# Optimization experiments

Hardware: AMD Instinct MI355X
Metric: run time of the kernel (lower is better)

Reference implementation:

```python
import jax, jax.numpy as jnp
import numpy as np

ROPE_BASE = 1000000.0
EPS = 1e-6
N_HEADS = 8


def apply_rope(x, base=ROPE_BASE):
    # x: [b, s, h, d]
    b, s, h, d = x.shape
    half = d // 2
    theta = 1.0 / base ** (2 * jnp.arange(half) / d)          # [half]
    angles = jnp.arange(s)[:, None] * theta[None, :]          # [s, half]
    cos = jnp.cos(angles)[None, :, None, :]                   # [1, s, 1, half]
    sin = jnp.sin(angles)[None, :, None, :]
    x1, x2 = jnp.split(x, 2, axis=-1)
    return jnp.concatenate([x1 * cos - x2 * sin, x1 * sin + x2 * cos], axis=-1)


def setup_inputs() -> dict:
    key = jax.random.key(0)
    ks = jax.random.split(key, 5)
    b, s, dim = 2, 4096, 512
    x = jax.random.normal(ks[0], (b, s, dim), dtype=jnp.float32)
    scale = jnp.ones((dim,), dtype=jnp.float32)
    init = 1.0 / np.sqrt(dim)
    Wq = jax.random.normal(ks[1], (dim, dim), dtype=jnp.float32) * init
    Wk = jax.random.normal(ks[2], (dim, dim), dtype=jnp.float32) * init
    Wv = jax.random.normal(ks[3], (dim, dim), dtype=jnp.float32) * init
    Wo = jax.random.normal(ks[4], (dim, dim), dtype=jnp.float32) * init
    return {"x": x, "scale": scale, "Wq": Wq, "Wk": Wk, "Wv": Wv, "Wo": Wo}


def reference(x, scale, Wq, Wk, Wv, Wo):
    b, s, dim = x.shape
    h = N_HEADS
    dh = dim // h
    # RMSNorm (use_fast_variance=False path)
    variance = jnp.mean(x ** 2, axis=-1, keepdims=True)
    x_norm = x / jnp.sqrt(variance + EPS) * scale
    # Projections (flax Linear: y = x @ kernel, kernel [in, out])
    q = (x_norm @ Wq).reshape(b, s, h, dh)
    k = (x_norm @ Wk).reshape(b, s, h, dh)
    v = (x_norm @ Wv).reshape(b, s, h, dh)
    q = apply_rope(q)
    k = apply_rope(k)
    scores = jnp.einsum('bthd,bshd->bhts', q, k) / jnp.sqrt(jnp.float32(dh))
    mask = jnp.triu(jnp.full((s, s), -jnp.inf, dtype=jnp.float32), k=1)
    scores = scores + mask[None, None, :, :]
    attn = jax.nn.softmax(scores, axis=-1)
    out = jnp.einsum('bhts,bshd->bthd', attn, v).reshape(b, s, dim)
    return out @ Wo
```

## Files before the change

### kernel.cpp

```cpp
#include <hip/hip_runtime.h>
#include <hip/hip_bf16.h>

typedef _Float16 f16;
typedef _Float16 f16x4 __attribute__((ext_vector_type(4)));
typedef _Float16 f16x8 __attribute__((ext_vector_type(8)));
typedef float f32x4 __attribute__((ext_vector_type(4)));

#define S_LEN 4096
#define DIM   512
#define NH    8
#define DH    64
#define BATCH 2
#define BHDIM (BATCH*NH)

#define QSCALE 0.18033688011112042f

__device__ __forceinline__ void gld16(const f16* g, f16* l) {
#if __has_builtin(__builtin_amdgcn_global_load_lds)
  __builtin_amdgcn_global_load_lds((const __attribute__((address_space(1))) void*)g,
                                   (__attribute__((address_space(3))) void*)l, 16, 0, 0);
#else
  *(f16x8*)l = *(const f16x8*)g;
#endif
}

__device__ __forceinline__ float fexp2(float x) {
#if __has_builtin(__builtin_amdgcn_exp2f)
  return __builtin_amdgcn_exp2f(x);
#else
  return exp2f(x);
#endif
}

__global__ __launch_bounds__(256) void rmsnorm_kernel(
    const float* __restrict__ x, const float* __restrict__ scale,
    f16* __restrict__ xn) {
  int row = blockIdx.x;
  int tid = threadIdx.x;
  const float* xr = x + (size_t)row * DIM;
  float2 v = *(const float2*)(xr + tid*2);
  float ss = v.x*v.x + v.y*v.y;
  #pragma unroll
  for (int off = 32; off > 0; off >>= 1) ss += __shfl_down(ss, off);
  __shared__ float red[4];
  if ((tid & 63) == 0) red[tid >> 6] = ss;
  __syncthreads();
  float tot = red[0] + red[1] + red[2] + red[3];
  float inv = rsqrtf(tot * (1.0f/DIM) + 1e-6f);
  float2 s = *(const float2*)(scale + tid*2);
  xn[(size_t)row*DIM + tid*2+0] = (f16)(v.x*inv*s.x);
  xn[(size_t)row*DIM + tid*2+1] = (f16)(v.y*inv*s.y);
}

__global__ void transpose_kernel(const float* __restrict__ Wq,
                                 const float* __restrict__ Wk,
                                 const float* __restrict__ Wv,
                                 const float* __restrict__ Wo,
                                 f16* __restrict__ wt_qkv, f16* __restrict__ wo_t) {
  __shared__ f16 tile[32][33];
  int mat = blockIdx.z;
  const float* src = (mat == 0) ? Wq : (mat == 1) ? Wk : (mat == 2) ? Wv : Wo;
  f16* dst = (mat < 3) ? (wt_qkv + (size_t)mat*DIM*DIM) : wo_t;
  int k0 = blockIdx.y * 32, n0 = blockIdx.x * 32;
  int tx = threadIdx.x, ty = threadIdx.y;
  #pragma unroll
  for (int i = 0; i < 32; i += 8)
    tile[ty+i][tx] = (f16)src[(size_t)(k0+ty+i)*DIM + n0+tx];
  __syncthreads();
  #pragma unroll
  for (int i = 0; i < 32; i += 8)
    dst[(size_t)(n0+ty+i)*DIM + k0+tx] = tile[tx][ty+i];
}

__global__ __launch_bounds__(256) void rope_table_kernel(float* __restrict__ ctab,
                                                         float* __restrict__ stab) {
  int idx = blockIdx.x*256 + threadIdx.x;
  int t = idx >> 5, d = idx & 31;
  float theta = exp2f(-(float)d * (19.931568569324174f / 32.0f));
  float sv, cv;
  sincosf((float)t * theta, &sv, &cv);
  ctab[idx] = cv; stab[idx] = sv;
}

__device__ __forceinline__ void gemm128_acc(
    const f16* __restrict__ A, const f16* __restrict__ Bt,
    int m0, int n0, f16* As, f16* Bs, f32x4 (&acc)[4][4]) {
  const int tid = threadIdx.x;
  const int wave = tid >> 6, lane = tid & 63;
  const int l16 = lane & 15, quad = lane >> 4;
  const int mrow = (wave & 1) * 64, ncol = (wave >> 1) * 64;
  const int srow = tid >> 3;
  const int gc = (tid & 7) ^ ((tid >> 3) & 7);

  for (int k0 = 0; k0 < DIM; k0 += 64) {
    if (k0) __syncthreads();
    #pragma unroll
    for (int i = 0; i < 4; i++) {
      gld16(A  + (size_t)(m0 + i*32 + srow)*DIM + k0 + gc*8, As + i*2048 + tid*8);
      gld16(Bt + (size_t)(n0 + i*32 + srow)*DIM + k0 + gc*8, Bs + i*2048 + tid*8);
    }
    __syncthreads();
    #pragma unroll
    for (int kc = 0; kc < 2; kc++) {
      f16x8 a[4], b[4];
      #pragma unroll
      for (int mt = 0; mt < 4; mt++) {
        int row = mrow + mt*16 + l16;
        a[mt] = *(const f16x8*)(As + row*64 + (((quad + 4*kc) ^ (l16 & 7)) * 8));
      }
      #pragma unroll
      for (int nt = 0; nt < 4; nt++) {
        int row = ncol + nt*16 + l16;
        b[nt] = *(const f16x8*)(Bs + row*64 + (((quad + 4*kc) ^ (l16 & 7)) * 8));
      }
      #pragma unroll
      for (int mt = 0; mt < 4; mt++)
        #pragma unroll
        for (int nt = 0; nt < 4; nt++)
          acc[mt][nt] = __builtin_amdgcn_mfma_f32_16x16x32_f16(a[mt], b[nt], acc[mt][nt], 0, 0, 0);
    }
  }
}

__global__ __launch_bounds__(256) void qkv_gemm_kernel(
    const f16* __restrict__ xn, const f16* __restrict__ wt,
    const float* __restrict__ ctab, const float* __restrict__ stab,
    f16* __restrict__ qbuf, f16* __restrict__ kbuf, f16* __restrict__ vt) {
  __shared__ __align__(16) f16 As[128*64], Bs[128*64];
  int m0 = blockIdx.x * 128, n0 = blockIdx.y * 128;
  f32x4 acc[4][4] = {};
  gemm128_acc(xn, wt, m0, n0, As, Bs, acc);

  const int tid = threadIdx.x;
  const int wave = tid >> 6, lane = tid & 63;
  const int l16 = lane & 15, quad = lane >> 4;
  int ncol = n0 + (wave >> 1) * 64;
  int which = ncol >> 9;
  int head = (ncol >> 6) & 7;
  int mbase = m0 + (wave & 1) * 64;

  if (which <= 1) {
    #pragma unroll
    for (int mt = 0; mt < 4; mt++)
      #pragma unroll
      for (int nt = 0; nt < 2; nt++) {
        int d = nt*16 + l16;
        #pragma unroll
        for (int r = 0; r < 4; r++) {
          int t = (mbase + mt*16 + quad*4 + r) & 4095;
          float cv = ctab[t*32 + d], sv = stab[t*32 + d];
          float x1 = acc[mt][nt][r], x2 = acc[mt][nt+2][r];
          acc[mt][nt][r]   = x1*cv - x2*sv;
          acc[mt][nt+2][r] = x1*sv + x2*cv;
        }
      }
  }
  if (which < 2) {
    float osc = (which == 0) ? QSCALE : 1.0f;
    f16* dst = which ? kbuf : qbuf;
    #pragma unroll
    for (int mt = 0; mt < 4; mt++)
      #pragma unroll
      for (int nt = 0; nt < 4; nt++)
        #pragma unroll
        for (int r = 0; r < 4; r++) {
          int m = mbase + mt*16 + quad*4 + r;
          int b = m >> 12, t = m & 4095;
          dst[(((size_t)(b*NH + head))*S_LEN + t)*DH + nt*16 + l16] = (f16)(acc[mt][nt][r]*osc);
        }
  } else {
    #pragma unroll
    for (int mt = 0; mt < 4; mt++)
      #pragma unroll
      for (int nt = 0; nt < 4; nt++) {
        int m = mbase + mt*16 + quad*4;
        int b = m >> 12, t = m & 4095;
        int d = nt*16 + l16;
        f16x4 v4 = {(f16)acc[mt][nt][0], (f16)acc[mt][nt][1],
                    (f16)acc[mt][nt][2], (f16)acc[mt][nt][3]};
        *(f16x4*)(vt + ((size_t)((b*NH + head)*DH + d))*S_LEN + t) = v4;
      }
  }
}

__global__ __launch_bounds__(128, 2) void attn_kernel(
    const f16* __restrict__ qbuf, const f16* __restrict__ kbuf,
    const f16* __restrict__ vtb, f16* __restrict__ ao) {
  int bid = blockIdx.x;
  int bh  = bid & 15;
  int p   = bid >> 4;

  int tid = threadIdx.x;
  int wave = tid >> 6, lane = tid & 63;
  int l16 = lane & 15, quad = lane >> 4;

  const f16* Q = qbuf + (size_t)bh*S_LEN*DH;
  const f16* K = kbuf + (size_t)bh*S_LEN*DH;
  const f16* V = vtb  + (size_t)bh*DH*S_LEN;

  int bandv[2] = {127 - p, p};
  int tcnt[2]  = {((127 - p) >> 1) + 1, (p >> 1) + 1};
  int rbase[2] = {bandv[0]*32 + wave*16, bandv[1]*32 + wave*16};

  f16x8 qa[2][2];
  #pragma unroll
  for (int bi = 0; bi < 2; bi++) {
    const f16* qrow = Q + (size_t)(rbase[bi] + l16)*DH + quad*8;
    qa[bi][0] = *(const f16x8*)(qrow);
    qa[bi][1] = *(const f16x8*)(qrow + 32);
  }

  f32x4 o[2][4] = {};
  float m_i[2] = {-1e30f, -1e30f};
  float l_i[2] = {0.f, 0.f};

  __shared__ __align__(16) f16 kt[2*4096];
  __shared__ __align__(16) f16 vs[2*4096];
  __shared__ __align__(16) f16 pls[4096];

  const int gcs = (tid & 7) ^ ((tid >> 3) & 7);
  const int srow = tid >> 3;

  #define STAGE(buf, kv)                                                        \
    do {                                                                        \
      f16* ktb = kt + (buf)*4096;                                               \
      f16* vsb = vs + (buf)*4096;                                               \
      _Pragma("unroll")                                                         \
      for (int n = 0; n < 4; n++) {                                             \
        gld16(K + (size_t)((kv) + n*16 + srow)*DH + gcs*8, ktb + n*1024 + tid*8);\
        gld16(V + (size_t)(n*16 + srow)*S_LEN + (kv) + gcs*8, vsb + n*1024 + tid*8);\
      }                                                                         \
    } while (0)

  STAGE(0, 0);
  __syncthreads();

  int nth = tcnt[0];
  for (int it = 0; it < nth; ++it) {
    int kv0 = it * 64;
    int cur = it & 1;
    if (it + 1 < nth) STAGE(cur ^ 1, kv0 + 64);

    const f16* ktc = kt + cur*4096;
    const f16* vsc = vs + cur*4096;

    bool act1 = (it < tcnt[1]);
    bool dia[2] = {it == tcnt[0] - 1, it == tcnt[1] - 1};

    #pragma unroll
    for (int bi = 0; bi < 2; bi++) {
      if (bi == 1 && !act1) continue;
      bool diag = dia[bi];
      int ntl = diag ? ((bandv[bi] & 1) ? 4 : 2) : 4;

      f32x4 st[4];
      #pragma unroll
      for (int nt = 0; nt < 4; nt++) {
        if (nt >= ntl) continue;
        int row = nt*16 + l16;
        f16x8 kf0 = *(const f16x8*)(ktc + row*64 + (((quad)     ^ (row & 7))*8));
        f16x8 kf1 = *(const f16x8*)(ktc + row*64 + (((quad + 4) ^ (row & 7))*8));
        f32x4 z = {};
        z = __builtin_amdgcn_mfma_f32_16x16x32_f16(kf0, qa[bi][0], z, 0, 0, 0);
        st[nt] = __builtin_amdgcn_mfma_f32_16x16x32_f16(kf1, qa[bi][1], z, 0, 0, 0);
      }

      int qglob = rbase[bi] + l16;
      float rmx = -1e30f;
      #pragma unroll
      for (int nt = 0; nt < 4; nt++) {
        if (nt >= ntl) continue;
        if (diag) {
          int kb = kv0 + nt*16 + quad*4;
          #pragma unroll
          for (int r = 0; r < 4; r++) {
            float v = st[nt][r];
            if (kb + r > qglob) v = -1e30f;
            st[nt][r] = v;
            rmx = fmaxf(rmx, v);
          }
        } else {
          #pragma unroll
          for (int r = 0; r < 4; r++) rmx = fmaxf(rmx, st[nt][r]);
        }
      }
      rmx = fmaxf(rmx, __shfl_xor(rmx, 16));
      rmx = fmaxf(rmx, __shfl_xor(rmx, 32));
      if (!__all(rmx <= m_i[bi] + 8.0f)) {
        float mnew = fmaxf(m_i[bi], rmx);
        float alpha = fexp2(m_i[bi] - mnew);
        m_i[bi] = mnew;
        float al[4];
        #pragma unroll
        for (int r = 0; r < 4; r++) al[r] = __shfl(alpha, quad*4 + r);
        #pragma unroll
        for (int dnt = 0; dnt < 4; dnt++)
          #pragma unroll
          for (int r = 0; r < 4; r++) o[bi][dnt][r] *= al[r];
        l_i[bi] *= alpha;
      }
      float mref = m_i[bi];
      float rs = 0.f;
      f16* plw = pls + wave*2048 + bi*1024 + l16*64;
      #pragma unroll
      for (int nt = 0; nt < 4; nt++) {
        if (nt >= ntl) continue;
        f16x4 p4;
        #pragma unroll
        for (int r = 0; r < 4; r++) {
          float pv = fexp2(st[nt][r] - mref);
          rs += pv;
          p4[r] = (f16)pv;
        }
        int cw = nt*2 + (quad >> 1);
        *(f16x4*)(plw + ((cw ^ (l16 & 7))*8) + (quad & 1)*4) = p4;
      }
      rs += __shfl_xor(rs, 16);
      rs += __shfl_xor(rs, 32);
      l_i[bi] += rs;
    }

    int kcl0 = dia[0] ? ((bandv[0] & 1) ? 2 : 1) : 2;
    int kcl1 = act1 ? (dia[1] ? ((bandv[1] & 1) ? 2 : 1) : 2) : 0;
    #pragma unroll
    for (int kc = 0; kc < 2; kc++) {
      bool lv0 = (kc < kcl0), lv1 = (kc < kcl1);
      if (!lv0 && !lv1) continue;
      int cp = ((kc*4 + quad) ^ (l16 & 7))*8;
      f16x8 pa0, pa1;
      if (lv0) pa0 = *(const f16x8*)(pls + wave*2048 +        l16*64 + cp);
      if (lv1) pa1 = *(const f16x8*)(pls + wave*2048 + 1024 + l16*64 + cp);
      #pragma unroll
      for (int dnt = 0; dnt < 4; dnt++) {
        int vr = dnt*16 + l16;
        f16x8 vf = *(const f16x8*)(vsc + vr*64 + (((kc*4 + quad) ^ (vr & 7))*8));
        if (lv0) o[0][dnt] = __builtin_amdgcn_mfma_f32_16x16x32_f16(pa0, vf, o[0][dnt], 0, 0, 0);
        if (lv1) o[1][dnt] = __builtin_amdgcn_mfma_f32_16x16x32_f16(pa1, vf, o[1][dnt], 0, 0, 0);
      }
    }

    __syncthreads();
  }
  #undef STAGE

  int b = bh >> 3, h = bh & 7;
  #pragma unroll
  for (int bi = 0; bi < 2; bi++) {
    float lr[4];
    #pragma unroll
    for (int r = 0; r < 4; r++) lr[r] = __shfl(l_i[bi], quad*4 + r);
    #pragma unroll
    for (int r = 0; r < 4; r++) {
      float invl = 1.0f / lr[r];
      int t = rbase[bi] + quad*4 + r;
      size_t rowoff = ((size_t)(b*S_LEN + t))*DIM + h*DH;
      #pragma unroll
      for (int dnt = 0; dnt < 4; dnt++)
        ao[rowoff + dnt*16 + l16] = (f16)(o[bi][dnt][r]*invl);
    }
  }
}

__global__ __launch_bounds__(256) void out_gemm_kernel(
    const f16* __restrict__ ao, const f16* __restrict__ wot,
    float* __restrict__ out) {
  __shared__ __align__(16) f16 As[128*64], Bs[128*64];
  int m0 = blockIdx.x * 128, n0 = blockIdx.y * 128;
  f32x4 acc[4][4] = {};
  gemm128_acc(ao, wot, m0, n0, As, Bs, acc);

  const int tid = threadIdx.x;
  const int wave = tid >> 6, lane = tid & 63;
  const int l16 = lane & 15, quad = lane >> 4;
  int ncol = n0 + (wave >> 1) * 64;
  int mbase = m0 + (wave & 1) * 64;
  #pragma unroll
  for (int mt = 0; mt < 4; mt++)
    #pragma unroll
    for (int nt = 0; nt < 4; nt++)
      #pragma unroll
      for (int r = 0; r < 4; r++)
        out[(size_t)(mbase + mt*16 + quad*4 + r)*DIM + ncol + nt*16 + l16] = acc[mt][nt][r];
}

extern "C" void kernel_launch(void* const* d_in, const int* in_sizes, int n_in,
                              void* d_out, int out_size, void* d_ws, size_t ws_size,
                              hipStream_t stream) {
  const float* x     = (const float*)d_in[0];
  const float* scale = (const float*)d_in[1];
  const float* Wq    = (const float*)d_in[2];
  const float* Wk    = (const float*)d_in[3];
  const float* Wv    = (const float*)d_in[4];
  const float* Wo    = (const float*)d_in[5];
  float* out = (float*)d_out;

  const size_t ROWS = (size_t)BATCH * S_LEN;
  char* ws = (char*)d_ws;
  f16* xn     = (f16*)ws;  ws += ROWS * DIM * sizeof(f16);
  f16* wt_qkv = (f16*)ws;  ws += (size_t)3 * DIM * DIM * sizeof(f16);
  f16* wo_t   = (f16*)ws;  ws += (size_t)DIM * DIM * sizeof(f16);
  f16* qb     = (f16*)ws;  ws += (size_t)BHDIM * S_LEN * DH * sizeof(f16);
  f16* kb     = (f16*)ws;  ws += (size_t)BHDIM * S_LEN * DH * sizeof(f16);
  f16* vt     = (f16*)ws;  ws += (size_t)BHDIM * S_LEN * DH * sizeof(f16);
  float* ctab = (float*)ws; ws += (size_t)S_LEN * 32 * sizeof(float);
  float* stab = (float*)ws; ws += (size_t)S_LEN * 32 * sizeof(float);
  f16* ao     = xn;

  size_t need = (size_t)(ws - (char*)d_ws);
  if (ws_size < need) return;

  rmsnorm_kernel   <<<ROWS, 256, 0, stream>>>(x, scale, xn);
  transpose_kernel <<<dim3(16,16,4), dim3(32,8), 0, stream>>>(Wq, Wk, Wv, Wo, wt_qkv, wo_t);
  rope_table_kernel<<<512, 256, 0, stream>>>(ctab, stab);
  qkv_gemm_kernel  <<<dim3(64,12), 256, 0, stream>>>(xn, wt_qkv, ctab, stab, qb, kb, vt);
  attn_kernel      <<<1024, 128, 0, stream>>>(qb, kb, vt, ao);
  out_gemm_kernel  <<<dim3(64,4), 256, 0, stream>>>(ao, wo_t, out);
}
```

Before: 211.0 us.

## Stage K/V through registers into single LDS buffer and raise occupancy

Replaces the double-buffered direct global-to-LDS K/V staging with register prefetch of the next tile, written into a single LDS buffer after the compute finishes. The P tile buffer is halved by running the PV product per band right after each softmax instead of after both bands. Together this shrinks shared memory so launch bounds can ask for 4 blocks per CU instead of 2. The trade-off is an extra barrier per iteration, more VGPR pressure from the prefetch registers, and less interleaving of the two bands' MFMAs.

```diff
diff --git a/kernel.cpp b/kernel.cpp
--- a/kernel.cpp
+++ b/kernel.cpp
@@ -183,7 +183,7 @@
   }
 }
 
-__global__ __launch_bounds__(128, 2) void attn_kernel(
+__global__ __launch_bounds__(128, 4) void attn_kernel(
     const f16* __restrict__ qbuf, const f16* __restrict__ kbuf,
     const f16* __restrict__ vtb, f16* __restrict__ ao) {
   int bid = blockIdx.x;
@@ -214,35 +214,36 @@
   float m_i[2] = {-1e30f, -1e30f};
   float l_i[2] = {0.f, 0.f};
 
-  __shared__ __align__(16) f16 kt[2*4096];
-  __shared__ __align__(16) f16 vs[2*4096];
-  __shared__ __align__(16) f16 pls[4096];
+  __shared__ __align__(16) f16 kt[4096];
+  __shared__ __align__(16) f16 vs[4096];
+  __shared__ __align__(16) f16 pls[2048];
 
   const int gcs = (tid & 7) ^ ((tid >> 3) & 7);
   const int srow = tid >> 3;
 
-  #define STAGE(buf, kv)                                                        \
-    do {                                                                        \
-      f16* ktb = kt + (buf)*4096;                                               \
-      f16* vsb = vs + (buf)*4096;                                               \
-      _Pragma("unroll")                                                         \
+  f16x8 pk[4], pvr[4];
+  #define LOADREG(kv)                                                           \
+    do { _Pragma("unroll")                                                      \
       for (int n = 0; n < 4; n++) {                                             \
-        gld16(K + (size_t)((kv) + n*16 + srow)*DH + gcs*8, ktb + n*1024 + tid*8);\
-        gld16(V + (size_t)(n*16 + srow)*S_LEN + (kv) + gcs*8, vsb + n*1024 + tid*8);\
-      }                                                                         \
-    } while (0)
-
-  STAGE(0, 0);
+        pk[n]  = *(const f16x8*)(K + (size_t)((kv) + n*16 + srow)*DH + gcs*8);  \
+        pvr[n] = *(const f16x8*)(V + (size_t)(n*16 + srow)*S_LEN + (kv) + gcs*8);\
+      } } while (0)
+  #define WRITELDS()                                                            \
+    do { _Pragma("unroll")                                                      \
+      for (int n = 0; n < 4; n++) {                                             \
+        *(f16x8*)(kt + n*1024 + tid*8) = pk[n];                                 \
+        *(f16x8*)(vs + n*1024 + tid*8) = pvr[n];                                \
+      } } while (0)
+
+  LOADREG(0);
+  WRITELDS();
   __syncthreads();
 
   int nth = tcnt[0];
   for (int it = 0; it < nth; ++it) {
     int kv0 = it * 64;
-    int cur = it & 1;
-    if (it + 1 < nth) STAGE(cur ^ 1, kv0 + 64);
-
-    const f16* ktc = kt + cur*4096;
-    const f16* vsc = vs + cur*4096;
+    bool have_next = (it + 1 < nth);
+    if (have_next) LOADREG(kv0 + 64);
 
     bool act1 = (it < tcnt[1]);
     bool dia[2] = {it == tcnt[0] - 1, it == tcnt[1] - 1};
@@ -258,8 +259,8 @@
       for (int nt = 0; nt < 4; nt++) {
         if (nt >= ntl) continue;
         int row = nt*16 + l16;
-        f16x8 kf0 = *(const f16x8*)(ktc + row*64 + (((quad)     ^ (row & 7))*8));
-        f16x8 kf1 = *(const f16x8*)(ktc + row*64 + (((quad + 4) ^ (row & 7))*8));
+        f16x8 kf0 = *(const f16x8*)(kt + row*64 + (((quad)     ^ (row & 7))*8));
+        f16x8 kf1 = *(const f16x8*)(kt + row*64 + (((quad + 4) ^ (row & 7))*8));
         f32x4 z = {};
         z = __builtin_amdgcn_mfma_f32_16x16x32_f16(kf0, qa[bi][0], z, 0, 0, 0);
         st[nt] = __builtin_amdgcn_mfma_f32_16x16x32_f16(kf1, qa[bi][1], z, 0, 0, 0);
@@ -301,7 +302,7 @@
       }
       float mref = m_i[bi];
       float rs = 0.f;
-      f16* plw = pls + wave*2048 + bi*1024 + l16*64;
+      f16* plw = pls + wave*1024 + l16*64;
       #pragma unroll
       for (int nt = 0; nt < 4; nt++) {
         if (nt >= ntl) continue;
@@ -318,30 +319,29 @@
       rs += __shfl_xor(rs, 16);
       rs += __shfl_xor(rs, 32);
       l_i[bi] += rs;
+
+      int kcl = diag ? ((bandv[bi] & 1) ? 2 : 1) : 2;
+      #pragma unroll
+      for (int kc = 0; kc < 2; kc++) {
+        if (kc >= kcl) continue;
+        f16x8 pa = *(const f16x8*)(plw - l16*64 + l16*64 + (((kc*4 + quad) ^ (l16 & 7))*8));
+        #pragma unroll
+        for (int dnt = 0; dnt < 4; dnt++) {
+          int vr = dnt*16 + l16;
+          f16x8 vf = *(const f16x8*)(vs + vr*64 + (((kc*4 + quad) ^ (vr & 7))*8));
+          o[bi][dnt] = __builtin_amdgcn_mfma_f32_16x16x32_f16(pa, vf, o[bi][dnt], 0, 0, 0);
+        }
+      }
     }
 
-    int kcl0 = dia[0] ? ((bandv[0] & 1) ? 2 : 1) : 2;
-    int kcl1 = act1 ? (dia[1] ? ((bandv[1] & 1) ? 2 : 1) : 2) : 0;
-    #pragma unroll
-    for (int kc = 0; kc < 2; kc++) {
-      bool lv0 = (kc < kcl0), lv1 = (kc < kcl1);
-      if (!lv0 && !lv1) continue;
-      int cp = ((kc*4 + quad) ^ (l16 & 7))*8;
-      f16x8 pa0, pa1;
-      if (lv0) pa0 = *(const f16x8*)(pls + wave*2048 +        l16*64 + cp);
-      if (lv1) pa1 = *(const f16x8*)(pls + wave*2048 + 1024 + l16*64 + cp);
-      #pragma unroll
-      for (int dnt = 0; dnt < 4; dnt++) {
-        int vr = dnt*16 + l16;
-        f16x8 vf = *(const f16x8*)(vsc + vr*64 + (((kc*4 + quad) ^ (vr & 7))*8));
-        if (lv0) o[0][dnt] = __builtin_amdgcn_mfma_f32_16x16x32_f16(pa0, vf, o[0][dnt], 0, 0, 0);
-        if (lv1) o[1][dnt] = __builtin_amdgcn_mfma_f32_16x16x32_f16(pa1, vf, o[1][dnt], 0, 0, 0);
-      }
+    if (have_next) {
+      __syncthreads();
+      WRITELDS();
+      __syncthreads();
     }
-
-    __syncthreads();
-  }
-  #undef STAGE
+  }
+  #undef LOADREG
+  #undef WRITELDS
 
   int b = bh >> 3, h = bh & 7;
   #pragma unroll
```

Result: slower. 545.1 us (+158.4%).

## Keep softmax probabilities in registers instead of round-tripping through LDS

Applied to the files above, without the earlier changes.

The P tile from the QK^T MFMA is now packed straight into registers (packed f16 conversion) and used as the A operand of the PV MFMA. It no longer goes through a shared-memory scratch buffer. To make the register layout match, the V fragment is gathered from LDS as two 4-element halves in a permuted k-order. The row-sum reduction across lanes is deferred to the epilogue. The QK^T loop is also merged across both bands so the K fragments load once. This removes LDS writes and reads and frees 8KB of LDS, at the cost of extra LDS read instructions for V, more register pressure, and round-toward-zero f16 conversion.

```diff
diff --git a/kernel.cpp b/kernel.cpp
--- a/kernel.cpp
+++ b/kernel.cpp
@@ -2,6 +2,7 @@
 #include <hip/hip_bf16.h>
 
 typedef _Float16 f16;
+typedef _Float16 f16x2 __attribute__((ext_vector_type(2)));
 typedef _Float16 f16x4 __attribute__((ext_vector_type(4)));
 typedef _Float16 f16x8 __attribute__((ext_vector_type(8)));
 typedef float f32x4 __attribute__((ext_vector_type(4)));
@@ -29,6 +30,16 @@
   return __builtin_amdgcn_exp2f(x);
 #else
   return exp2f(x);
+#endif
+}
+
+__device__ __forceinline__ f16x2 pk2(float a, float b) {
+#if __has_builtin(__builtin_amdgcn_cvt_pkrtz)
+  auto r = __builtin_amdgcn_cvt_pkrtz(a, b);
+  f16x2 o; __builtin_memcpy(&o, &r, sizeof(o));
+  return o;
+#else
+  f16x2 r; r[0] = (f16)a; r[1] = (f16)b; return r;
 #endif
 }
 
@@ -216,7 +227,6 @@
 
   __shared__ __align__(16) f16 kt[2*4096];
   __shared__ __align__(16) f16 vs[2*4096];
-  __shared__ __align__(16) f16 pls[4096];
 
   const int gcs = (tid & 7) ^ ((tid >> 3) & 7);
   const int srow = tid >> 3;
@@ -245,26 +255,37 @@
     const f16* vsc = vs + cur*4096;
 
     bool act1 = (it < tcnt[1]);
-    bool dia[2] = {it == tcnt[0] - 1, it == tcnt[1] - 1};
-
-    #pragma unroll
-    for (int bi = 0; bi < 2; bi++) {
-      if (bi == 1 && !act1) continue;
-      bool diag = dia[bi];
-      int ntl = diag ? ((bandv[bi] & 1) ? 4 : 2) : 4;
-
-      f32x4 st[4];
-      #pragma unroll
-      for (int nt = 0; nt < 4; nt++) {
-        if (nt >= ntl) continue;
+    bool dia0 = (it == tcnt[0] - 1), dia1 = (it == tcnt[1] - 1);
+    int ntl0 = dia0 ? ((bandv[0] & 1) ? 4 : 2) : 4;
+    int ntl1 = act1 ? (dia1 ? ((bandv[1] & 1) ? 4 : 2) : 4) : 0;
+
+    f32x4 st[2][4];
+    #pragma unroll
+    for (int nt = 0; nt < 4; nt++) {
+      bool n0 = (nt < ntl0), n1 = (nt < ntl1);
+      if (n0 || n1) {
         int row = nt*16 + l16;
         f16x8 kf0 = *(const f16x8*)(ktc + row*64 + (((quad)     ^ (row & 7))*8));
         f16x8 kf1 = *(const f16x8*)(ktc + row*64 + (((quad + 4) ^ (row & 7))*8));
-        f32x4 z = {};
-        z = __builtin_amdgcn_mfma_f32_16x16x32_f16(kf0, qa[bi][0], z, 0, 0, 0);
-        st[nt] = __builtin_amdgcn_mfma_f32_16x16x32_f16(kf1, qa[bi][1], z, 0, 0, 0);
-      }
-
+        if (n0) {
+          f32x4 z = {};
+          z = __builtin_amdgcn_mfma_f32_16x16x32_f16(kf0, qa[0][0], z, 0, 0, 0);
+          st[0][nt] = __builtin_amdgcn_mfma_f32_16x16x32_f16(kf1, qa[0][1], z, 0, 0, 0);
+        }
+        if (n1) {
+          f32x4 z = {};
+          z = __builtin_amdgcn_mfma_f32_16x16x32_f16(kf0, qa[1][0], z, 0, 0, 0);
+          st[1][nt] = __builtin_amdgcn_mfma_f32_16x16x32_f16(kf1, qa[1][1], z, 0, 0, 0);
+        }
+      }
+    }
+
+    f16x8 pa[2][2];
+    #pragma unroll
+    for (int bi = 0; bi < 2; bi++) {
+      int ntl = bi ? ntl1 : ntl0;
+      if (ntl == 0) continue;
+      bool diag = bi ? dia1 : dia0;
       int qglob = rbase[bi] + l16;
       float rmx = -1e30f;
       #pragma unroll
@@ -274,14 +295,14 @@
           int kb = kv0 + nt*16 + quad*4;
           #pragma unroll
           for (int r = 0; r < 4; r++) {
-            float v = st[nt][r];
+            float v = st[bi][nt][r];
             if (kb + r > qglob) v = -1e30f;
-            st[nt][r] = v;
+            st[bi][nt][r] = v;
             rmx = fmaxf(rmx, v);
           }
         } else {
           #pragma unroll
-          for (int r = 0; r < 4; r++) rmx = fmaxf(rmx, st[nt][r]);
+          for (int r = 0; r < 4; r++) rmx = fmaxf(rmx, st[bi][nt][r]);
         }
       }
       rmx = fmaxf(rmx, __shfl_xor(rmx, 16));
@@ -300,42 +321,42 @@
         l_i[bi] *= alpha;
       }
       float mref = m_i[bi];
+      int kcl = ntl >> 1;
       float rs = 0.f;
-      f16* plw = pls + wave*2048 + bi*1024 + l16*64;
-      #pragma unroll
-      for (int nt = 0; nt < 4; nt++) {
-        if (nt >= ntl) continue;
-        f16x4 p4;
-        #pragma unroll
-        for (int r = 0; r < 4; r++) {
-          float pv = fexp2(st[nt][r] - mref);
-          rs += pv;
-          p4[r] = (f16)pv;
-        }
-        int cw = nt*2 + (quad >> 1);
-        *(f16x4*)(plw + ((cw ^ (l16 & 7))*8) + (quad & 1)*4) = p4;
-      }
-      rs += __shfl_xor(rs, 16);
-      rs += __shfl_xor(rs, 32);
+      #pragma unroll
+      for (int c = 0; c < 2; c++) {
+        if (c >= kcl) continue;
+        float e0 = fexp2(st[bi][2*c  ][0] - mref);
+        float e1 = fexp2(st[bi][2*c  ][1] - mref);
+        float e2 = fexp2(st[bi][2*c  ][2] - mref);
+        float e3 = fexp2(st[bi][2*c  ][3] - mref);
+        float e4 = fexp2(st[bi][2*c+1][0] - mref);
+        float e5 = fexp2(st[bi][2*c+1][1] - mref);
+        float e6 = fexp2(st[bi][2*c+1][2] - mref);
+        float e7 = fexp2(st[bi][2*c+1][3] - mref);
+        rs += ((e0+e1)+(e2+e3)) + ((e4+e5)+(e6+e7));
+        f16x4 h0 = __builtin_shufflevector(pk2(e0,e1), pk2(e2,e3), 0,1,2,3);
+        f16x4 h1 = __builtin_shufflevector(pk2(e4,e5), pk2(e6,e7), 0,1,2,3);
+        pa[bi][c] = __builtin_shufflevector(h0, h1, 0,1,2,3,4,5,6,7);
+      }
       l_i[bi] += rs;
     }
 
-    int kcl0 = dia[0] ? ((bandv[0] & 1) ? 2 : 1) : 2;
-    int kcl1 = act1 ? (dia[1] ? ((bandv[1] & 1) ? 2 : 1) : 2) : 0;
-    #pragma unroll
-    for (int kc = 0; kc < 2; kc++) {
-      bool lv0 = (kc < kcl0), lv1 = (kc < kcl1);
+    int kcl0 = ntl0 >> 1, kcl1 = ntl1 >> 1;
+    #pragma unroll
+    for (int c = 0; c < 2; c++) {
+      bool lv0 = (c < kcl0), lv1 = (c < kcl1);
       if (!lv0 && !lv1) continue;
-      int cp = ((kc*4 + quad) ^ (l16 & 7))*8;
-      f16x8 pa0, pa1;
-      if (lv0) pa0 = *(const f16x8*)(pls + wave*2048 +        l16*64 + cp);
-      if (lv1) pa1 = *(const f16x8*)(pls + wave*2048 + 1024 + l16*64 + cp);
       #pragma unroll
       for (int dnt = 0; dnt < 4; dnt++) {
         int vr = dnt*16 + l16;
-        f16x8 vf = *(const f16x8*)(vsc + vr*64 + (((kc*4 + quad) ^ (vr & 7))*8));
-        if (lv0) o[0][dnt] = __builtin_amdgcn_mfma_f32_16x16x32_f16(pa0, vf, o[0][dnt], 0, 0, 0);
-        if (lv1) o[1][dnt] = __builtin_amdgcn_mfma_f32_16x16x32_f16(pa1, vf, o[1][dnt], 0, 0, 0);
+        int iLo = vr*64 + (((c*4 +     (quad>>1)) ^ (vr & 7))*8) + (quad & 1)*4;
+        int iHi = vr*64 + (((c*4 + 2 + (quad>>1)) ^ (vr & 7))*8) + (quad & 1)*4;
+        f16x4 lo = *(const f16x4*)(vsc + iLo);
+        f16x4 hi = *(const f16x4*)(vsc + iHi);
+        f16x8 vf = __builtin_shufflevector(lo, hi, 0,1,2,3,4,5,6,7);
+        if (lv0) o[0][dnt] = __builtin_amdgcn_mfma_f32_16x16x32_f16(pa[0][c], vf, o[0][dnt], 0, 0, 0);
+        if (lv1) o[1][dnt] = __builtin_amdgcn_mfma_f32_16x16x32_f16(pa[1][c], vf, o[1][dnt], 0, 0, 0);
       }
     }
 
@@ -346,9 +367,12 @@
   int b = bh >> 3, h = bh & 7;
   #pragma unroll
   for (int bi = 0; bi < 2; bi++) {
+    float lf = l_i[bi];
+    lf += __shfl_xor(lf, 16);
+    lf += __shfl_xor(lf, 32);
     float lr[4];
     #pragma unroll
-    for (int r = 0; r < 4; r++) lr[r] = __shfl(l_i[bi], quad*4 + r);
+    for (int r = 0; r < 4; r++) lr[r] = __shfl(lf, quad*4 + r);
     #pragma unroll
     for (int r = 0; r < 4; r++) {
       float invl = 1.0f / lr[r];
```

New measurement: 205.5 us. 1.03x faster.
